# Kernel tuning notes

Hardware: AMD Instinct MI355X
Metric: run time of the kernel (lower is better)

## Reference

```python
import jax, jax.numpy as jnp
import numpy as np

B, N, D, H = 2, 2048, 1024, 16
HD = D // H
SCALE = HD ** -0.5


def setup_inputs() -> dict:
    key = jax.random.key(0)
    ks = jax.random.split(key, 9)
    s = D ** -0.5
    return {
        "x": jax.random.normal(ks[0], (B, N, D), dtype=jnp.float32),
        "Wq": jax.random.normal(ks[1], (D, D), dtype=jnp.float32) * s,
        "bq": jax.random.normal(ks[2], (D,), dtype=jnp.float32) * 0.01,
        "Wk": jax.random.normal(ks[3], (D, D), dtype=jnp.float32) * s,
        "bk": jax.random.normal(ks[4], (D,), dtype=jnp.float32) * 0.01,
        "Wv": jax.random.normal(ks[5], (D, D), dtype=jnp.float32) * s,
        "bv": jax.random.normal(ks[6], (D,), dtype=jnp.float32) * 0.01,
        "Wo": jax.random.normal(ks[7], (D, D), dtype=jnp.float32) * s,
        "bo": jax.random.normal(ks[8], (D,), dtype=jnp.float32) * 0.01,
    }


def reference(x, Wq, bq, Wk, bk, Wv, bv, Wo, bo):
    # Q/K/V projections (torch Linear: x @ W.T + b), split into heads: (B,H,N,HD)
    def proj(W, b):
        return (x @ W.T + b).reshape(B, N, H, HD).transpose(0, 2, 1, 3)

    q = proj(Wq, bq)
    k = proj(Wk, bk)
    v = proj(Wv, bv)
    # Scaled dot-product attention with explicit (B,H,N,N) scores
    scores = jnp.einsum("bhnd,bhmd->bhnm", q, k) * SCALE
    attn = jax.nn.softmax(scores, axis=-1)
    y = jnp.einsum("bhnm,bhmd->bhnd", attn, v)
    y = y.transpose(0, 2, 1, 3).reshape(B, N, D)
    # Output projection
    return y @ Wo.T + bo
```

## Files before the change

kernel.cpp:

```cpp
#include <hip/hip_runtime.h>

#define BB 2
#define NN 2048
#define DD 1024
#define HH 16
#define HD 64
#define SCALE 0.125f

typedef unsigned short u16;
typedef unsigned int u32;
typedef __attribute__((ext_vector_type(8))) short short8;
typedef __attribute__((ext_vector_type(4))) float float4v;

__device__ __forceinline__ float b2f(u16 u) {
    union { float f; u32 i; } x; x.i = ((u32)u) << 16; return x.f;
}
__device__ __forceinline__ u16 f2b(float f) {
    union { float f; u32 i; } x; x.f = f;
    u32 i = x.i;
    return (u16)((i + 0x7fffu + ((i >> 16) & 1u)) >> 16);
}

__device__ __forceinline__ void gl_lds16(const u16* g, u16* l) {
    __builtin_amdgcn_global_load_lds(
        (__attribute__((address_space(1))) void*)(void*)g,
        (__attribute__((address_space(3))) void*)l, 16, 0, 0);
}

__global__ __launch_bounds__(256) void cvt_x(
    const float* __restrict__ s, u16* __restrict__ d)
{
    int i = (blockIdx.x * 256 + threadIdx.x) * 8;
    float4v a = *(const float4v*)(s + i);
    float4v b = *(const float4v*)(s + i + 4);
    short8 r;
    r[0] = (short)f2b(a[0]); r[1] = (short)f2b(a[1]);
    r[2] = (short)f2b(a[2]); r[3] = (short)f2b(a[3]);
    r[4] = (short)f2b(b[0]); r[5] = (short)f2b(b[1]);
    r[6] = (short)f2b(b[2]); r[7] = (short)f2b(b[3]);
    *(short8*)(d + i) = r;
}

__global__ __launch_bounds__(256) void cvt_w4(
    const float* __restrict__ Wq, const float* __restrict__ Wk,
    const float* __restrict__ Wv, const float* __restrict__ Wo,
    u16* __restrict__ d4)
{
    const int which = blockIdx.y;
    const float* s = (which == 0) ? Wq : (which == 1) ? Wk : (which == 2) ? Wv : Wo;
    u16* d = d4 + (size_t)which * 1048576;
    int i = (blockIdx.x * 256 + threadIdx.x) * 8;
    float4v a = *(const float4v*)(s + i);
    float4v b = *(const float4v*)(s + i + 4);
    short8 r;
    r[0] = (short)f2b(a[0]); r[1] = (short)f2b(a[1]);
    r[2] = (short)f2b(a[2]); r[3] = (short)f2b(a[3]);
    r[4] = (short)f2b(b[0]); r[5] = (short)f2b(b[1]);
    r[6] = (short)f2b(b[2]); r[7] = (short)f2b(b[3]);
    *(short8*)(d + i) = r;
}


__global__ __launch_bounds__(256) void gemm_qkv(
    const u16* __restrict__ xb,
    const u16* __restrict__ Wqb, const float* __restrict__ bq,
    const u16* __restrict__ Wkb, const float* __restrict__ bk,
    const u16* __restrict__ Wvb, const float* __restrict__ bv,
    u16* __restrict__ Qo, u16* __restrict__ Ko, u16* __restrict__ Vt)
{
    const int tm = blockIdx.y;
    const int tn_all = blockIdx.x;
    const int mat = tn_all >> 3;
    const int tn = tn_all & 7;

    const u16* __restrict__ W     = (mat == 0) ? Wqb : (mat == 1) ? Wkb : Wvb;
    const float* __restrict__ bias = (mat == 0) ? bq : (mat == 1) ? bk : bv;

    __shared__ u16 As[128 * 32];
    __shared__ u16 Bs[128 * 32];

    const int tid  = threadIdx.x;
    const int wave = tid >> 6, lane = tid & 63;
    const int wm = wave >> 1, wn = wave & 1;
    const int quad = lane >> 4, l16 = lane & 15;

    const int r0 = tid >> 2, c0 = tid & 3;
    const int r1 = r0 + 64;

    const u16* ga0 = &xb[(size_t)(tm * 128 + r0) * DD + c0 * 8];
    const u16* ga1 = &xb[(size_t)(tm * 128 + r1) * DD + c0 * 8];
    const u16* gb0 = &W [(size_t)(tn * 128 + r0) * DD + c0 * 8];
    const u16* gb1 = &W [(size_t)(tn * 128 + r1) * DD + c0 * 8];

    float4v acc[4][4] = {};

    for (int k0 = 0; k0 < DD; k0 += 32) {
        __syncthreads();
        gl_lds16(ga0 + k0, &As[tid * 8]);
        gl_lds16(ga1 + k0, &As[(256 + tid) * 8]);
        gl_lds16(gb0 + k0, &Bs[tid * 8]);
        gl_lds16(gb1 + k0, &Bs[(256 + tid) * 8]);
        asm volatile("s_waitcnt vmcnt(0)" ::: "memory");
        __syncthreads();

        short8 af[4], bf[4];
        #pragma unroll
        for (int mi = 0; mi < 4; ++mi)
            af[mi] = *(const short8*)&As[(wm * 64 + mi * 16 + l16) * 32 + quad * 8];
        #pragma unroll
        for (int ni = 0; ni < 4; ++ni)
            bf[ni] = *(const short8*)&Bs[(wn * 64 + ni * 16 + l16) * 32 + quad * 8];

        #pragma unroll
        for (int mi = 0; mi < 4; ++mi)
            #pragma unroll
            for (int ni = 0; ni < 4; ++ni)
                acc[mi][ni] = __builtin_amdgcn_mfma_f32_16x16x32_bf16(
                    af[mi], bf[ni], acc[mi][ni], 0, 0, 0);
    }

    #pragma unroll
    for (int mi = 0; mi < 4; ++mi) {
        #pragma unroll
        for (int ni = 0; ni < 4; ++ni) {
            int cc = tn * 128 + wn * 64 + ni * 16 + l16;
            int h = cc >> 6, hd = cc & 63;
            float bv_ = bias[cc];
            #pragma unroll
            for (int rr = 0; rr < 4; ++rr) {
                int R = tm * 128 + wm * 64 + mi * 16 + quad * 4 + rr;
                int b = R >> 11, n = R & 2047;
                u16 val = f2b(acc[mi][ni][rr] + bv_);
                if (mat == 2) {
                    Vt[(((size_t)(b * HH + h)) * HD + hd) * NN + n] = val;
                } else {
                    u16* Out = (mat == 0) ? Qo : Ko;
                    Out[(((size_t)(b * HH + h)) * NN + n) * HD + hd] = val;
                }
            }
        }
    }
}

__global__ __launch_bounds__(256) void gemm_out(
    const u16* __restrict__ A, const u16* __restrict__ W,
    const float* __restrict__ bias, float* __restrict__ Out)
{
    const int tm = blockIdx.y;
    const int tn = blockIdx.x;

    __shared__ u16 As[128 * 32];
    __shared__ u16 Bs[128 * 32];

    const int tid  = threadIdx.x;
    const int wave = tid >> 6, lane = tid & 63;
    const int wm = wave >> 1, wn = wave & 1;
    const int quad = lane >> 4, l16 = lane & 15;

    const int r0 = tid >> 2, c0 = tid & 3;
    const int r1 = r0 + 64;

    const u16* ga0 = &A[(size_t)(tm * 128 + r0) * DD + c0 * 8];
    const u16* ga1 = &A[(size_t)(tm * 128 + r1) * DD + c0 * 8];
    const u16* gb0 = &W[(size_t)(tn * 128 + r0) * DD + c0 * 8];
    const u16* gb1 = &W[(size_t)(tn * 128 + r1) * DD + c0 * 8];

    float4v acc[4][4] = {};

    for (int k0 = 0; k0 < DD; k0 += 32) {
        __syncthreads();
        gl_lds16(ga0 + k0, &As[tid * 8]);
        gl_lds16(ga1 + k0, &As[(256 + tid) * 8]);
        gl_lds16(gb0 + k0, &Bs[tid * 8]);
        gl_lds16(gb1 + k0, &Bs[(256 + tid) * 8]);
        asm volatile("s_waitcnt vmcnt(0)" ::: "memory");
        __syncthreads();

        short8 af[4], bf[4];
        #pragma unroll
        for (int mi = 0; mi < 4; ++mi)
            af[mi] = *(const short8*)&As[(wm * 64 + mi * 16 + l16) * 32 + quad * 8];
        #pragma unroll
        for (int ni = 0; ni < 4; ++ni)
            bf[ni] = *(const short8*)&Bs[(wn * 64 + ni * 16 + l16) * 32 + quad * 8];

        #pragma unroll
        for (int mi = 0; mi < 4; ++mi)
            #pragma unroll
            for (int ni = 0; ni < 4; ++ni)
                acc[mi][ni] = __builtin_amdgcn_mfma_f32_16x16x32_bf16(
                    af[mi], bf[ni], acc[mi][ni], 0, 0, 0);
    }

    #pragma unroll
    for (int mi = 0; mi < 4; ++mi) {
        #pragma unroll
        for (int ni = 0; ni < 4; ++ni) {
            int cc = tn * 128 + wn * 64 + ni * 16 + l16;
            float bv_ = bias[cc];
            #pragma unroll
            for (int rr = 0; rr < 4; ++rr) {
                int R = tm * 128 + wm * 64 + mi * 16 + quad * 4 + rr;
                Out[(size_t)R * DD + cc] = acc[mi][ni][rr] + bv_;
            }
        }
    }
}

__global__ __launch_bounds__(256, 2) void attn_mfma(
    const u16* __restrict__ Q, const u16* __restrict__ K,
    const u16* __restrict__ Vt, u16* __restrict__ Y)
{
    const int qb = blockIdx.x;
    const int bh = blockIdx.y;
    const int tid = threadIdx.x;
    const int wave = tid >> 6, lane = tid & 63;
    const int quad = lane >> 4, l16 = lane & 15;

    const u16* __restrict__ Qb = Q + (size_t)bh * NN * HD;
    const u16* __restrict__ Kb = K + (size_t)bh * NN * HD;
    const u16* __restrict__ Vb = Vt + (size_t)bh * HD * NN;

    __shared__ u16 Ks[64 * 72];
    __shared__ u16 Vs[64 * 72];
    __shared__ u16 Ps[4][16 * 72];

    short8 qa[2][2];
    #pragma unroll
    for (int g = 0; g < 2; ++g) {
        int qrow = qb * 128 + wave * 32 + g * 16 + l16;
        #pragma unroll
        for (int kc = 0; kc < 2; ++kc) {
            short8 t = *(const short8*)&Qb[(size_t)qrow * HD + kc * 32 + quad * 8];
            #pragma unroll
            for (int j = 0; j < 8; ++j)
                qa[g][kc][j] = (short)f2b(b2f((u16)t[j]) * SCALE);
        }
    }

    short8 onesB;
    #pragma unroll
    for (int j = 0; j < 8; ++j) onesB[j] = (short)0x3F80;

    float4v oc[2][4] = {};
    float4v la[2] = {};

    const int kkey = tid >> 2, koct = tid & 3;
    const int vhd  = tid >> 3, vko  = tid & 7;

    short8 kreg[2], vreg[2];
    kreg[0] = *(const short8*)&Kb[(size_t)kkey * HD + koct * 8];
    kreg[1] = *(const short8*)&Kb[(size_t)kkey * HD + (koct + 4) * 8];
    vreg[0] = *(const short8*)&Vb[(size_t)vhd * NN + vko * 8];
    vreg[1] = *(const short8*)&Vb[(size_t)(vhd + 32) * NN + vko * 8];

    for (int k0 = 0; k0 < NN; k0 += 64) {
        __syncthreads();
        *(short8*)&Ks[kkey * 72 + koct * 8] = kreg[0];
        *(short8*)&Ks[kkey * 72 + (koct + 4) * 8] = kreg[1];
        *(short8*)&Vs[vhd * 72 + vko * 8] = vreg[0];
        *(short8*)&Vs[(vhd + 32) * 72 + vko * 8] = vreg[1];
        __syncthreads();

        int k1 = k0 + 64;
        if (k1 < NN) {
            kreg[0] = *(const short8*)&Kb[(size_t)(k1 + kkey) * HD + koct * 8];
            kreg[1] = *(const short8*)&Kb[(size_t)(k1 + kkey) * HD + (koct + 4) * 8];
            vreg[0] = *(const short8*)&Vb[(size_t)vhd * NN + k1 + vko * 8];
            vreg[1] = *(const short8*)&Vb[(size_t)(vhd + 32) * NN + k1 + vko * 8];
        }

        short8 kb[4][2], vb[4][2];
        #pragma unroll
        for (int kt = 0; kt < 4; ++kt)
            #pragma unroll
            for (int kc = 0; kc < 2; ++kc)
                kb[kt][kc] = *(const short8*)&Ks[(kt * 16 + l16) * 72 + kc * 32 + quad * 8];
        #pragma unroll
        for (int ht = 0; ht < 4; ++ht)
            #pragma unroll
            for (int kc = 0; kc < 2; ++kc)
                vb[ht][kc] = *(const short8*)&Vs[(ht * 16 + l16) * 72 + kc * 32 + quad * 8];

        #pragma unroll
        for (int g = 0; g < 2; ++g) {
            float4v sc[4];
            #pragma unroll
            for (int kt = 0; kt < 4; ++kt) {
                float4v z = {};
                z = __builtin_amdgcn_mfma_f32_16x16x32_bf16(qa[g][0], kb[kt][0], z, 0, 0, 0);
                sc[kt] = __builtin_amdgcn_mfma_f32_16x16x32_bf16(qa[g][1], kb[kt][1], z, 0, 0, 0);
            }

            #pragma unroll
            for (int rr = 0; rr < 4; ++rr) {
                #pragma unroll
                for (int kt = 0; kt < 4; ++kt) {
                    float p = __expf(sc[kt][rr] - 8.0f);
                    union { float f; u32 i; } px; px.f = p;
                    Ps[wave][(quad * 4 + rr) * 72 + kt * 16 + l16] = (u16)(px.i >> 16);
                }
            }
            asm volatile("s_waitcnt lgkmcnt(0)" ::: "memory");

            short8 pa0 = *(const short8*)&Ps[wave][l16 * 72 + quad * 8];
            short8 pa1 = *(const short8*)&Ps[wave][l16 * 72 + 32 + quad * 8];

            la[g] = __builtin_amdgcn_mfma_f32_16x16x32_bf16(pa0, onesB, la[g], 0, 0, 0);
            la[g] = __builtin_amdgcn_mfma_f32_16x16x32_bf16(pa1, onesB, la[g], 0, 0, 0);
            #pragma unroll
            for (int ht = 0; ht < 4; ++ht) {
                oc[g][ht] = __builtin_amdgcn_mfma_f32_16x16x32_bf16(pa0, vb[ht][0], oc[g][ht], 0, 0, 0);
                oc[g][ht] = __builtin_amdgcn_mfma_f32_16x16x32_bf16(pa1, vb[ht][1], oc[g][ht], 0, 0, 0);
            }
        }
    }

    const int b = bh >> 4, h = bh & 15;
    #pragma unroll
    for (int g = 0; g < 2; ++g) {
        #pragma unroll
        for (int ht = 0; ht < 4; ++ht) {
            #pragma unroll
            for (int rr = 0; rr < 4; ++rr) {
                int n = qb * 128 + wave * 32 + g * 16 + quad * 4 + rr;
                int col = h * HD + ht * 16 + l16;
                Y[((size_t)(b * NN + n)) * DD + col] = f2b(oc[g][ht][rr] / la[g][rr]);
            }
        }
    }
}

extern "C" void kernel_launch(void* const* d_in, const int* in_sizes, int n_in,
                              void* d_out, int out_size, void* d_ws, size_t ws_size,
                              hipStream_t stream) {
    const float* x  = (const float*)d_in[0];
    const float* Wq = (const float*)d_in[1];
    const float* bq = (const float*)d_in[2];
    const float* Wk = (const float*)d_in[3];
    const float* bk = (const float*)d_in[4];
    const float* Wv = (const float*)d_in[5];
    const float* bv = (const float*)d_in[6];
    const float* Wo = (const float*)d_in[7];
    const float* bo = (const float*)d_in[8];
    float* out = (float*)d_out;

    const size_t M1 = 1024 * 1024;
    u16* base = (u16*)d_ws;
    u16* xb  = base;
    u16* W4  = base + 4 * M1;
    u16* Wqb = W4;
    u16* Wkb = W4 + 1 * M1;
    u16* Wvb = W4 + 2 * M1;
    u16* Wob = W4 + 3 * M1;
    u16* Qw  = base + 8 * M1;
    u16* Kw  = base + 12 * M1;
    u16* Vtw = base + 16 * M1;
    u16* Yw  = xb;

    cvt_x<<<dim3(2048), 256, 0, stream>>>(x, xb);
    cvt_w4<<<dim3(512, 4), 256, 0, stream>>>(Wq, Wk, Wv, Wo, W4);

    gemm_qkv<<<dim3(24, 32), 256, 0, stream>>>(xb, Wqb, bq, Wkb, bk, Wvb, bv,
                                               Qw, Kw, Vtw);

    attn_mfma<<<dim3(16, 32), 256, 0, stream>>>(Qw, Kw, Vtw, Yw);

    gemm_out<<<dim3(8, 32), 256, 0, stream>>>(Yw, Wob, bo, out);
}
```

Measured before the change: 215.0 us.

## Restructure attention to direct-to-LDS loads, smaller query tiles, and merged convert kernel

The attention kernel now handles 64 query rows per block instead of 128 and doubles the grid. K/V tiles go straight into LDS with global_load_lds, using an XOR-style rotation swizzle in place of row padding, which drops the register-staged prefetch. Launch bounds rise to allow 4 blocks per CU. The two fp32-to-bf16 convert kernels become one launch. The change aims for higher occupancy and fewer register round-trips, but it gives up the overlap of the next tile's load with compute because each iteration waits on vmcnt(0), and each K/V tile is reused by fewer queries.

```diff
diff --git a/kernel.cpp b/kernel.cpp
--- a/kernel.cpp
+++ b/kernel.cpp
@@ -27,37 +27,31 @@
         (__attribute__((address_space(3))) void*)l, 16, 0, 0);
 }
 
-__global__ __launch_bounds__(256) void cvt_x(
-    const float* __restrict__ s, u16* __restrict__ d)
+__global__ __launch_bounds__(256) void cvt_all(
+    const float* __restrict__ x,
+    const float* __restrict__ Wq, const float* __restrict__ Wk,
+    const float* __restrict__ Wv, const float* __restrict__ Wo,
+    u16* __restrict__ xb, u16* __restrict__ W4)
 {
-    int i = (blockIdx.x * 256 + threadIdx.x) * 8;
-    float4v a = *(const float4v*)(s + i);
-    float4v b = *(const float4v*)(s + i + 4);
+    int e = (blockIdx.x * 256 + threadIdx.x) * 8;
+    const float* s;
+    u16* d;
+    if (e < 4194304) { s = x + e; d = xb + e; }
+    else {
+        int e2 = e - 4194304;
+        int which = e2 >> 20;
+        int off = e2 & 1048575;
+        s = ((which == 0) ? Wq : (which == 1) ? Wk : (which == 2) ? Wv : Wo) + off;
+        d = W4 + e2;
+    }
+    float4v a = *(const float4v*)s;
+    float4v b = *(const float4v*)(s + 4);
     short8 r;
     r[0] = (short)f2b(a[0]); r[1] = (short)f2b(a[1]);
     r[2] = (short)f2b(a[2]); r[3] = (short)f2b(a[3]);
     r[4] = (short)f2b(b[0]); r[5] = (short)f2b(b[1]);
     r[6] = (short)f2b(b[2]); r[7] = (short)f2b(b[3]);
-    *(short8*)(d + i) = r;
-}
-
-__global__ __launch_bounds__(256) void cvt_w4(
-    const float* __restrict__ Wq, const float* __restrict__ Wk,
-    const float* __restrict__ Wv, const float* __restrict__ Wo,
-    u16* __restrict__ d4)
-{
-    const int which = blockIdx.y;
-    const float* s = (which == 0) ? Wq : (which == 1) ? Wk : (which == 2) ? Wv : Wo;
-    u16* d = d4 + (size_t)which * 1048576;
-    int i = (blockIdx.x * 256 + threadIdx.x) * 8;
-    float4v a = *(const float4v*)(s + i);
-    float4v b = *(const float4v*)(s + i + 4);
-    short8 r;
-    r[0] = (short)f2b(a[0]); r[1] = (short)f2b(a[1]);
-    r[2] = (short)f2b(a[2]); r[3] = (short)f2b(a[3]);
-    r[4] = (short)f2b(b[0]); r[5] = (short)f2b(b[1]);
-    r[6] = (short)f2b(b[2]); r[7] = (short)f2b(b[3]);
-    *(short8*)(d + i) = r;
+    *(short8*)d = r;
 }
 
 
@@ -207,7 +201,7 @@
     }
 }
 
-__global__ __launch_bounds__(256, 2) void attn_mfma(
+__global__ __launch_bounds__(256, 4) void attn_mfma(
     const u16* __restrict__ Q, const u16* __restrict__ K,
     const u16* __restrict__ Vt, u16* __restrict__ Y)
 {
@@ -221,20 +215,19 @@
     const u16* __restrict__ Kb = K + (size_t)bh * NN * HD;
     const u16* __restrict__ Vb = Vt + (size_t)bh * HD * NN;
 
-    __shared__ u16 Ks[64 * 72];
-    __shared__ u16 Vs[64 * 72];
+    __shared__ u16 Ks[64 * 64];
+    __shared__ u16 Vs[64 * 64];
     __shared__ u16 Ps[4][16 * 72];
 
-    short8 qa[2][2];
-    #pragma unroll
-    for (int g = 0; g < 2; ++g) {
-        int qrow = qb * 128 + wave * 32 + g * 16 + l16;
+    short8 qa[2];
+    {
+        int qrow = qb * 64 + wave * 16 + l16;
         #pragma unroll
         for (int kc = 0; kc < 2; ++kc) {
             short8 t = *(const short8*)&Qb[(size_t)qrow * HD + kc * 32 + quad * 8];
             #pragma unroll
             for (int j = 0; j < 8; ++j)
-                qa[g][kc][j] = (short)f2b(b2f((u16)t[j]) * SCALE);
+                qa[kc][j] = (short)f2b(b2f((u16)t[j]) * SCALE);
         }
     }
 
@@ -242,91 +235,68 @@
     #pragma unroll
     for (int j = 0; j < 8; ++j) onesB[j] = (short)0x3F80;
 
-    float4v oc[2][4] = {};
-    float4v la[2] = {};
-
-    const int kkey = tid >> 2, koct = tid & 3;
-    const int vhd  = tid >> 3, vko  = tid & 7;
-
-    short8 kreg[2], vreg[2];
-    kreg[0] = *(const short8*)&Kb[(size_t)kkey * HD + koct * 8];
-    kreg[1] = *(const short8*)&Kb[(size_t)kkey * HD + (koct + 4) * 8];
-    vreg[0] = *(const short8*)&Vb[(size_t)vhd * NN + vko * 8];
-    vreg[1] = *(const short8*)&Vb[(size_t)(vhd + 32) * NN + vko * 8];
+    float4v oc[4] = {};
+    float4v la = {};
+
+    const int srow = tid >> 3, sslot = tid & 7;
+    const int oA = (sslot + srow) & 7;
+    const int oB = (sslot + srow + 32) & 7;
+
+    const int fs0 = ((quad - l16) & 7) * 8;
+    const int fs1 = ((4 + quad - l16) & 7) * 8;
 
     for (int k0 = 0; k0 < NN; k0 += 64) {
         __syncthreads();
-        *(short8*)&Ks[kkey * 72 + koct * 8] = kreg[0];
-        *(short8*)&Ks[kkey * 72 + (koct + 4) * 8] = kreg[1];
-        *(short8*)&Vs[vhd * 72 + vko * 8] = vreg[0];
-        *(short8*)&Vs[(vhd + 32) * 72 + vko * 8] = vreg[1];
-        __syncthreads();
-
-        int k1 = k0 + 64;
-        if (k1 < NN) {
-            kreg[0] = *(const short8*)&Kb[(size_t)(k1 + kkey) * HD + koct * 8];
-            kreg[1] = *(const short8*)&Kb[(size_t)(k1 + kkey) * HD + (koct + 4) * 8];
-            vreg[0] = *(const short8*)&Vb[(size_t)vhd * NN + k1 + vko * 8];
-            vreg[1] = *(const short8*)&Vb[(size_t)(vhd + 32) * NN + k1 + vko * 8];
-        }
-
-        short8 kb[4][2], vb[4][2];
-        #pragma unroll
-        for (int kt = 0; kt < 4; ++kt)
-            #pragma unroll
-            for (int kc = 0; kc < 2; ++kc)
-                kb[kt][kc] = *(const short8*)&Ks[(kt * 16 + l16) * 72 + kc * 32 + quad * 8];
-        #pragma unroll
-        for (int ht = 0; ht < 4; ++ht)
-            #pragma unroll
-            for (int kc = 0; kc < 2; ++kc)
-                vb[ht][kc] = *(const short8*)&Vs[(ht * 16 + l16) * 72 + kc * 32 + quad * 8];
-
-        #pragma unroll
-        for (int g = 0; g < 2; ++g) {
-            float4v sc[4];
+        gl_lds16(&Kb[(size_t)(k0 + srow) * HD + oA * 8],        &Ks[tid * 8]);
+        gl_lds16(&Kb[(size_t)(k0 + srow + 32) * HD + oB * 8],   &Ks[(256 + tid) * 8]);
+        gl_lds16(&Vb[(size_t)srow * NN + k0 + oA * 8],          &Vs[tid * 8]);
+        gl_lds16(&Vb[(size_t)(srow + 32) * NN + k0 + oB * 8],   &Vs[(256 + tid) * 8]);
+        asm volatile("s_waitcnt vmcnt(0)" ::: "memory");
+        __syncthreads();
+
+        float4v sc[4];
+        #pragma unroll
+        for (int kt = 0; kt < 4; ++kt) {
+            short8 kb0 = *(const short8*)&Ks[(kt * 16 + l16) * 64 + fs0];
+            short8 kb1 = *(const short8*)&Ks[(kt * 16 + l16) * 64 + fs1];
+            float4v z = {};
+            z = __builtin_amdgcn_mfma_f32_16x16x32_bf16(qa[0], kb0, z, 0, 0, 0);
+            sc[kt] = __builtin_amdgcn_mfma_f32_16x16x32_bf16(qa[1], kb1, z, 0, 0, 0);
+        }
+
+        #pragma unroll
+        for (int rr = 0; rr < 4; ++rr) {
             #pragma unroll
             for (int kt = 0; kt < 4; ++kt) {
-                float4v z = {};
-                z = __builtin_amdgcn_mfma_f32_16x16x32_bf16(qa[g][0], kb[kt][0], z, 0, 0, 0);
-                sc[kt] = __builtin_amdgcn_mfma_f32_16x16x32_bf16(qa[g][1], kb[kt][1], z, 0, 0, 0);
+                float p = __expf(sc[kt][rr] - 8.0f);
+                union { float f; u32 i; } px; px.f = p;
+                Ps[wave][(quad * 4 + rr) * 72 + kt * 16 + l16] = (u16)(px.i >> 16);
             }
-
-            #pragma unroll
-            for (int rr = 0; rr < 4; ++rr) {
-                #pragma unroll
-                for (int kt = 0; kt < 4; ++kt) {
-                    float p = __expf(sc[kt][rr] - 8.0f);
-                    union { float f; u32 i; } px; px.f = p;
-                    Ps[wave][(quad * 4 + rr) * 72 + kt * 16 + l16] = (u16)(px.i >> 16);
-                }
-            }
-            asm volatile("s_waitcnt lgkmcnt(0)" ::: "memory");
-
-            short8 pa0 = *(const short8*)&Ps[wave][l16 * 72 + quad * 8];
-            short8 pa1 = *(const short8*)&Ps[wave][l16 * 72 + 32 + quad * 8];
-
-            la[g] = __builtin_amdgcn_mfma_f32_16x16x32_bf16(pa0, onesB, la[g], 0, 0, 0);
-            la[g] = __builtin_amdgcn_mfma_f32_16x16x32_bf16(pa1, onesB, la[g], 0, 0, 0);
-            #pragma unroll
-            for (int ht = 0; ht < 4; ++ht) {
-                oc[g][ht] = __builtin_amdgcn_mfma_f32_16x16x32_bf16(pa0, vb[ht][0], oc[g][ht], 0, 0, 0);
-                oc[g][ht] = __builtin_amdgcn_mfma_f32_16x16x32_bf16(pa1, vb[ht][1], oc[g][ht], 0, 0, 0);
-            }
+        }
+        asm volatile("s_waitcnt lgkmcnt(0)" ::: "memory");
+
+        short8 pa0 = *(const short8*)&Ps[wave][l16 * 72 + quad * 8];
+        short8 pa1 = *(const short8*)&Ps[wave][l16 * 72 + 32 + quad * 8];
+
+        la = __builtin_amdgcn_mfma_f32_16x16x32_bf16(pa0, onesB, la, 0, 0, 0);
+        la = __builtin_amdgcn_mfma_f32_16x16x32_bf16(pa1, onesB, la, 0, 0, 0);
+        #pragma unroll
+        for (int ht = 0; ht < 4; ++ht) {
+            short8 vb0 = *(const short8*)&Vs[(ht * 16 + l16) * 64 + fs0];
+            short8 vb1 = *(const short8*)&Vs[(ht * 16 + l16) * 64 + fs1];
+            oc[ht] = __builtin_amdgcn_mfma_f32_16x16x32_bf16(pa0, vb0, oc[ht], 0, 0, 0);
+            oc[ht] = __builtin_amdgcn_mfma_f32_16x16x32_bf16(pa1, vb1, oc[ht], 0, 0, 0);
         }
     }
 
     const int b = bh >> 4, h = bh & 15;
     #pragma unroll
-    for (int g = 0; g < 2; ++g) {
-        #pragma unroll
-        for (int ht = 0; ht < 4; ++ht) {
-            #pragma unroll
-            for (int rr = 0; rr < 4; ++rr) {
-                int n = qb * 128 + wave * 32 + g * 16 + quad * 4 + rr;
-                int col = h * HD + ht * 16 + l16;
-                Y[((size_t)(b * NN + n)) * DD + col] = f2b(oc[g][ht][rr] / la[g][rr]);
-            }
+    for (int ht = 0; ht < 4; ++ht) {
+        #pragma unroll
+        for (int rr = 0; rr < 4; ++rr) {
+            int n = qb * 64 + wave * 16 + quad * 4 + rr;
+            int col = h * HD + ht * 16 + l16;
+            Y[((size_t)(b * NN + n)) * DD + col] = f2b(oc[ht][rr] / la[rr]);
         }
     }
 }
@@ -358,13 +328,12 @@
     u16* Vtw = base + 16 * M1;
     u16* Yw  = xb;
 
-    cvt_x<<<dim3(2048), 256, 0, stream>>>(x, xb);
-    cvt_w4<<<dim3(512, 4), 256, 0, stream>>>(Wq, Wk, Wv, Wo, W4);
+    cvt_all<<<dim3(4096), 256, 0, stream>>>(x, Wq, Wk, Wv, Wo, xb, W4);
 
     gemm_qkv<<<dim3(24, 32), 256, 0, stream>>>(xb, Wqb, bq, Wkb, bk, Wvb, bv,
                                                Qw, Kw, Vtw);
 
-    attn_mfma<<<dim3(16, 32), 256, 0, stream>>>(Qw, Kw, Vtw, Yw);
+    attn_mfma<<<dim3(32, 32), 256, 0, stream>>>(Qw, Kw, Vtw, Yw);
 
     gemm_out<<<dim3(8, 32), 256, 0, stream>>>(Yw, Wob, bo, out);
 }
```

After: 212.0 us. Within noise of the previous version (-1.4%).
